# Kernel tuning notes

Hardware: AMD Instinct MI355X
Metric: run time of the kernel (lower is better)

Reference implementation:

```python
import jax, jax.numpy as jnp
import numpy as np

B, L, D = 4, 2048, 512
CHUNK = 64
EPS = 1e-5


def setup_inputs() -> dict:
    key = jax.random.key(0)
    kx, kw = jax.random.split(key)
    x = jax.random.normal(kx, (B, L, D), dtype=jnp.float32)
    W = jax.random.normal(kw, (D, D), dtype=jnp.float32) / np.float32(np.sqrt(D))
    return {
        "x": x,
        "W": W,
        "eta": jnp.asarray(0.01, jnp.float32),
        "lam_logit": jnp.asarray(np.log(0.99 / 0.01), jnp.float32),  # logit(0.99)
        "ln_gamma": jnp.ones((D,), jnp.float32),
        "ln_beta": jnp.zeros((D,), jnp.float32),
    }


def _gated_delta_scan(k, v, q, lam, beta):
    """Gated delta rule: S_t = lam*S_{t-1} + beta * k_t (x) (v_t - lam*S_{t-1}^T k_t);
    o_t = S_t^T q_t (scale=1.0, single head of dim D). k,v,q: [B,L,D] -> o: [B,L,D]."""
    b, l, d = k.shape
    nc = l // CHUNK

    def to_scan(t):  # [B,L,D] -> [nc, CHUNK, B, D]
        return t.transpose(1, 0, 2).reshape(nc, CHUNK, b, d)

    ks, vs, qs = to_scan(k), to_scan(v), to_scan(q)

    def step(S, inp):
        k_t, v_t, q_t = inp                      # each [B,D]
        S = lam * S                              # scalar decay exp(g), g = log(lam)
        v_err = beta * (v_t - jnp.einsum('bk,bkv->bv', k_t, S))
        S = S + k_t[:, :, None] * v_err[:, None, :]
        o_t = jnp.einsum('bk,bkv->bv', q_t, S)
        return S, o_t

    def chunk_body(S, ch):
        return jax.lax.scan(step, S, ch)

    S0 = jnp.zeros((b, d, d), k.dtype)
    _, o = jax.lax.scan(chunk_body, S0, (ks, vs, qs))  # o: [nc, CHUNK, B, D]
    return o.reshape(l, b, d).transpose(1, 0, 2)


def reference(x, W, eta, lam_logit, ln_gamma, ln_beta):
    lam = jax.nn.sigmoid(lam_logit)
    x_act = jnp.tanh(x)
    static_out = jnp.einsum('bld,ed->ble', x_act, W)  # torch Linear (no bias): x @ W.T
    # k = q = tanh(x), v = W @ tanh(x), g = log(lam), beta = eta
    o_dyn = _gated_delta_scan(x_act, static_out, x_act, lam, eta)
    y = static_out + o_dyn
    mu = jnp.mean(y, axis=-1, keepdims=True)
    var = jnp.var(y, axis=-1, keepdims=True)
    return (y - mu) * jax.lax.rsqrt(var + EPS) * ln_gamma + ln_beta
```

## Files before the change

### kernel.cpp

```cpp
#include <hip/hip_runtime.h>
#include <math.h>

#define BB 4
#define LL 2048
#define DD 512
#define CC 64
#define NC 32
#define VB 8
#define EPSF 1e-5f

typedef unsigned int u32;
typedef unsigned short u16;
typedef __attribute__((ext_vector_type(4))) u32 u32x4;
typedef __attribute__((ext_vector_type(4))) float f32x4;
typedef __attribute__((ext_vector_type(8))) __bf16 bf16x8;

__device__ __forceinline__ u16 f2bf(float f) {
  return __builtin_bit_cast(u16, (__bf16)f);
}
__device__ __forceinline__ int sx6(int s) { return (s ^ (s >> 3)) & 7; }
__device__ __forceinline__ bf16x8 ldf(const u16* p) {
  return __builtin_bit_cast(bf16x8, *(const u32x4*)p);
}
__device__ __forceinline__ bf16x8 bcv(u32x4 v) { return __builtin_bit_cast(bf16x8, v); }

__device__ __forceinline__ void gld16(u16* lds, const u16* g) {
  __builtin_amdgcn_global_load_lds(
      (const __attribute__((address_space(1))) u32*)g,
      (__attribute__((address_space(3))) u32*)lds, 16, 0, 0);
}
__device__ __forceinline__ void barrier_lgkm() {
  asm volatile("s_waitcnt lgkmcnt(0)" ::: "memory");
  __builtin_amdgcn_sched_barrier(0);
  __builtin_amdgcn_s_barrier();
  __builtin_amdgcn_sched_barrier(0);
}
__device__ __forceinline__ void barrier_all() {
  asm volatile("s_waitcnt vmcnt(0) lgkmcnt(0)" ::: "memory");
  __builtin_amdgcn_sched_barrier(0);
  __builtin_amdgcn_s_barrier();
  __builtin_amdgcn_sched_barrier(0);
}

__global__ __launch_bounds__(256) void k_cvtW(const float* __restrict__ W,
                                              u16* __restrict__ wbb) {
  int idx = (blockIdx.x * 256 + threadIdx.x) * 8;
  float4 a = *(const float4*)(W + idx);
  float4 b = *(const float4*)(W + idx + 4);
  float v[8] = {a.x, a.y, a.z, a.w, b.x, b.y, b.z, b.w};
  u32x4 pk;
#pragma unroll
  for (int j = 0; j < 4; ++j)
    pk[j] = (u32)f2bf(v[2 * j]) | ((u32)f2bf(v[2 * j + 1]) << 16);
  *(u32x4*)(wbb + idx) = pk;
}

__global__ __launch_bounds__(256) void k_prep3(const float* __restrict__ x,
                                               const float* __restrict__ eta_p,
                                               const float* __restrict__ ll_p,
                                               u16* __restrict__ kbs,
                                               u16* __restrict__ tbs,
                                               u16* __restrict__ tcs,
                                               u16* __restrict__ p1g,
                                               u16* __restrict__ p2g,
                                               u16* __restrict__ kbt) {
  __shared__ __align__(16) u16 Kl[CC * DD];
  __shared__ float Gl[64 * 64];
  __shared__ float Gs[64 * 64];
  __shared__ float Tl[64 * 65];
  __shared__ __align__(16) u16 MtL[64 * 64];
  __shared__ __align__(16) u16 TbT[64 * 64];
  __shared__ __align__(16) u16 TcT[64 * 64];
  __shared__ float pw[72];
  int bc = blockIdx.x;
  int b = bc >> 5, c = bc & 31;
  int tid = threadIdx.x;
  int wid = tid >> 6, lane = tid & 63;
  int lo = lane & 15, hi = lane >> 4;
  float beta = *eta_p;
  float lam = 1.f / (1.f + expf(-*ll_p));
  if (tid <= 64) pw[tid] = powf(lam, (float)tid);
  for (int i = tid; i < 64 * 65; i += 256) Tl[i] = 0.f;
  const float* xg = x + (size_t)(b * LL + c * CC) * DD;
  u16* kbs_c = kbs + (size_t)(b * LL + c * CC) * DD;
#pragma unroll
  for (int i = 0; i < 16; ++i) {
    int idx = tid + i * 256;
    int r = idx >> 6, k8 = (idx & 63) * 8;
    const float* xp = xg + (size_t)r * DD + k8;
    float4 a = *(const float4*)xp;
    float4 b4 = *(const float4*)(xp + 4);
    float v[8] = {a.x, a.y, a.z, a.w, b4.x, b4.y, b4.z, b4.w};
    u32x4 pk;
#pragma unroll
    for (int j = 0; j < 4; ++j)
      pk[j] = (u32)f2bf(tanhf(v[2 * j])) | ((u32)f2bf(tanhf(v[2 * j + 1])) << 16);
    int off = r * DD + (k8 ^ (sx6(r) << 3));
    *(u32x4*)(Kl + off) = pk;
    *(u32x4*)(kbs_c + off) = pk;
  }
  __syncthreads();
  {
    f32x4 acc[4] = {{0.f,0.f,0.f,0.f},{0.f,0.f,0.f,0.f},{0.f,0.f,0.f,0.f},{0.f,0.f,0.f,0.f}};
    int t = 16 * wid + lo;
    int mT = sx6(t) << 3;
#pragma unroll
    for (int kq = 0; kq < 16; ++kq) {
      int col = hi * 8 + kq * 32;
      bf16x8 aF = ldf(Kl + t * DD + (col ^ mT));
#pragma unroll
      for (int sb = 0; sb < 4; ++sb) {
        int s = 16 * sb + lo;
        bf16x8 bF = ldf(Kl + s * DD + (col ^ (sx6(s) << 3)));
        acc[sb] = __builtin_amdgcn_mfma_f32_16x16x32_bf16(aF, bF, acc[sb], 0, 0, 0);
      }
    }
#pragma unroll
    for (int sb = 0; sb < 4; ++sb)
#pragma unroll
      for (int r = 0; r < 4; ++r)
        Gl[(16 * wid + 4 * hi + r) * 64 + 16 * sb + lo] = acc[sb][r];
  }
  __syncthreads();
#pragma unroll
  for (int i = 0; i < 16; ++i) {
    int idx = tid + i * 256;
    int tq = idx >> 6, sq = idx & 63;
    Gs[idx] = (sq < tq) ? beta * pw[tq - sq] * Gl[idx] : 0.f;
  }
  __syncthreads();
  {
    int q = hi;
    int j = 16 * wid + lo;
    for (int t = 0; t < 64; ++t) {
      float ps = 0.f;
#pragma unroll
      for (int i = 0; i < 16; ++i) {
        int s = 16 * q + i;
        ps = fmaf(Gs[t * 64 + s], Tl[s * 65 + j], ps);
      }
      ps += __shfl_xor(ps, 16, 64);
      ps += __shfl_xor(ps, 32, 64);
      if (q == 0) Tl[t * 65 + j] = ((t == j) ? 1.f : 0.f) - ps;
    }
  }
  __syncthreads();
  u16* tbso = tbs + (size_t)bc * 4096;
  u16* tcso = tcs + (size_t)bc * 4096;
#pragma unroll
  for (int i = 0; i < 16; ++i) {
    int idx = tid + i * 256;
    int s = idx >> 6, r = idx & 63;
    float tv = Tl[s * 65 + r];
    float sc = pw[63 - s] * beta;
    tbso[idx] = f2bf(sc * tv);
    tcso[idx] = f2bf(-sc * pw[r + 1] * tv);
    int swz = r ^ (sx6(s) << 3);
    float mtv = (r < s) ? pw[s - r] * Gl[s * 64 + r]
                        : ((r == s) ? Gl[s * 64 + r] : 0.f);
    MtL[s * 64 + swz] = f2bf(mtv);
    float tvT = Tl[r * 65 + s];
    TbT[s * 64 + swz] = f2bf(beta * tvT);
    TcT[s * 64 + swz] = f2bf(-beta * pw[s + 1] * tvT);
  }
  __syncthreads();
  {
    f32x4 p1a[4], p2a[4];
#pragma unroll
    for (int rt = 0; rt < 4; ++rt) {
      p1a[rt] = (f32x4){0.f, 0.f, 0.f, 0.f};
      p2a[rt] = (f32x4){0.f, 0.f, 0.f, 0.f};
    }
    int srow = 16 * wid + lo;
    int aswz = sx6(srow) << 3;
#pragma unroll
    for (int km = 0; km < 2; ++km) {
      int mo = hi * 8 + km * 32;
      bf16x8 aF = ldf(MtL + srow * 64 + (mo ^ aswz));
#pragma unroll
      for (int rt = 0; rt < 4; ++rt) {
        int rrow = 16 * rt + lo;
        int bswz = sx6(rrow) << 3;
        p1a[rt] = __builtin_amdgcn_mfma_f32_16x16x32_bf16(
            aF, ldf(TbT + rrow * 64 + (mo ^ bswz)), p1a[rt], 0, 0, 0);
        p2a[rt] = __builtin_amdgcn_mfma_f32_16x16x32_bf16(
            aF, ldf(TcT + rrow * 64 + (mo ^ bswz)), p2a[rt], 0, 0, 0);
      }
    }
    u16* p1o = p1g + (size_t)bc * 4096;
    u16* p2o = p2g + (size_t)bc * 4096;
#pragma unroll
    for (int rt = 0; rt < 4; ++rt)
#pragma unroll
      for (int rg = 0; rg < 4; ++rg) {
        int s = 16 * wid + 4 * hi + rg;
        int r = 16 * rt + lo;
        float d1 = (s == r) ? 1.f : 0.f;
        float d2 = (s == r) ? pw[s + 1] : 0.f;
        p1o[s * 64 + r] = f2bf(p1a[rt][rg] + d1);
        p2o[s * 64 + r] = f2bf(p2a[rt][rg] + d2);
      }
  }
  u16* ktb = kbt + (size_t)bc * CC * DD;
#pragma unroll
  for (int rr = 0; rr < 2; ++rr) {
    int k = rr * 256 + tid;
    int kbase = k & ~7, klo = k & 7;
    int mk = sx6(k) << 3;
#pragma unroll
    for (int g = 0; g < 8; ++g) {
      u32 w4[4];
#pragma unroll
      for (int p = 0; p < 4; ++p) {
        int s0 = g * 8 + 2 * p;
        u16 e0 = Kl[s0 * DD + (kbase ^ (sx6(s0) << 3)) + klo];
        u16 e1 = Kl[(s0 + 1) * DD + (kbase ^ (sx6(s0 + 1) << 3)) + klo];
        w4[p] = (u32)e0 | ((u32)e1 << 16);
      }
      *(u32x4*)(ktb + (size_t)k * 64 + ((8 * g) ^ mk)) = (u32x4){w4[0], w4[1], w4[2], w4[3]};
    }
  }
}

__global__ __launch_bounds__(512, 2) void k_scanC(const u16* __restrict__ kbs,
                                                  const u16* __restrict__ kbt,
                                                  const u16* __restrict__ wbb,
                                                  const u16* __restrict__ tbs,
                                                  const u16* __restrict__ tcs,
                                                  const u16* __restrict__ p1g,
                                                  const u16* __restrict__ p2g,
                                                  const float* __restrict__ ll_p,
                                                  float* __restrict__ y) {
  __shared__ __align__(16) u16 Sb[16 * DD];
  __shared__ __align__(16) u16 Ut2[2][16 * 64];
  __shared__ __align__(16) u16 Vt2[2][16 * 64];
  __shared__ __align__(16) u16 Ws[16 * 64];

  int b = blockIdx.x >> 6;
  int vb = blockIdx.x & 63;
  int v0 = vb * VB;
  int tid = threadIdx.x;
  int wid = tid >> 6, lane = tid & 63;
  int wq = wid & 3, kh = wid >> 2;
  int lo = lane & 15, hi = lane >> 4;
  int sidx = 16 * wq + lo;
  int mS = sx6(sidx) << 3;
  int mLo = sx6(lo) << 3;
  int kOff = kh * 256;

  float lam = 1.f / (1.f + expf(-*ll_p));
  float lam64 = powf(lam, 64.f);

  {
    u32x4 z = {0u, 0u, 0u, 0u};
    ((u32x4*)Sb)[tid] = z;
    if (tid < 256) {
      ((u32x4*)Ut2)[tid] = z;
      ((u32x4*)Vt2)[tid] = z;
    }
    if (tid < 128) ((u32x4*)Ws)[tid] = z;
    if (wid < 8 && wid >= 0) {}
    if (wid < 8) {
      u32x4 wrow = *(const u32x4*)(wbb + (size_t)(v0 + wid) * DD + lane * 8);
      *(u32x4*)(Sb + (size_t)(8 + wid) * DD + ((lane * 8) ^ (sx6(8 + wid) << 3))) = wrow;
    }
  }
  const u16* kb_b = kbs + (size_t)b * LL * DD;
  float* yb = y + (size_t)b * LL * DD;

  u32x4 kB[8];
#pragma unroll
  for (int kq = 0; kq < 8; ++kq)
    kB[kq] = *(const u32x4*)(kb_b + (size_t)sidx * DD +
                             ((kOff + hi * 8 + kq * 32) ^ mS));
  u32x4 kt0[4], kt1[4], fA0, fA1, fB0, fB1;
  {
    const u16* ktc = kbt + (size_t)(b * NC + 0) * CC * DD;
#pragma unroll
    for (int t = 0; t < 4; ++t) {
      int k = 16 * (4 * wid + t) + lo;
      const u16* rowp = ktc + (size_t)k * 64;
      int m = sx6(k) << 3;
      kt0[t] = *(const u32x4*)(rowp + ((8 * hi) ^ m));
      kt1[t] = *(const u32x4*)(rowp + ((8 * hi + 32) ^ m));
    }
    size_t tbase = ((size_t)(b * NC + 0) * 64 + sidx) * 64 + hi * 8;
    const u16* mA = (kh == 0) ? tbs : p1g;
    const u16* mB = (kh == 0) ? tcs : p2g;
    fA0 = *(const u32x4*)(mA + tbase);
    fA1 = *(const u32x4*)(mA + tbase + 32);
    fB0 = *(const u32x4*)(mB + tbase);
    fB1 = *(const u32x4*)(mB + tbase + 32);
  }
  f32x4 Sa[4];
#pragma unroll
  for (int t = 0; t < 4; ++t) Sa[t] = (f32x4){0.f, 0.f, 0.f, 0.f};
  barrier_all();

  for (int c = 0; c < NC; ++c) {
    {
      f32x4 A0 = {0.f,0.f,0.f,0.f}, A1 = {0.f,0.f,0.f,0.f};
#pragma unroll
      for (int kq = 0; kq < 8; ++kq) {
        int col = kOff + hi * 8 + kq * 32;
        bf16x8 sA = ldf(Sb + lo * DD + (col ^ mLo));
        if (kq & 1) A1 = __builtin_amdgcn_mfma_f32_16x16x32_bf16(sA, bcv(kB[kq]), A1, 0, 0, 0);
        else        A0 = __builtin_amdgcn_mfma_f32_16x16x32_bf16(sA, bcv(kB[kq]), A0, 0, 0, 0);
      }
      f32x4 F = A0 + A1;
      if (hi < 2) {
#pragma unroll
        for (int r = 0; r < 4; ++r) {
          int m = 4 * hi + r;
          Ut2[kh][m * 64 + (sidx ^ (sx6(m) << 3))] = f2bf(F[r]);
        }
      } else {
#pragma unroll
        for (int r = 0; r < 4; ++r) {
          int m = 4 * hi + r - 8;
          Vt2[kh][m * 64 + (sidx ^ (sx6(m) << 3))] = f2bf(F[r]);
        }
      }
    }
    if (c + 1 < NC) {
      const u16* src = kb_b + ((size_t)(c + 1) * CC + sidx) * DD;
#pragma unroll
      for (int kq = 0; kq < 8; ++kq)
        kB[kq] = *(const u32x4*)(src + ((kOff + hi * 8 + kq * 32) ^ mS));
    }
    barrier_lgkm();
    {
      f32x4 Wa0 = {0.f,0.f,0.f,0.f}, Wa1 = {0.f,0.f,0.f,0.f};
#pragma unroll
      for (int h = 0; h < 2; ++h) {
        bf16x8 vf0 = ldf(Vt2[h] + lo * 64 + ((hi * 8) ^ mLo));
        bf16x8 vf1 = ldf(Vt2[h] + lo * 64 + ((hi * 8 + 32) ^ mLo));
        bf16x8 uf0 = ldf(Ut2[h] + lo * 64 + ((hi * 8) ^ mLo));
        bf16x8 uf1 = ldf(Ut2[h] + lo * 64 + ((hi * 8 + 32) ^ mLo));
        Wa0 = __builtin_amdgcn_mfma_f32_16x16x32_bf16(vf0, bcv(fA0), Wa0, 0, 0, 0);
        Wa1 = __builtin_amdgcn_mfma_f32_16x16x32_bf16(vf1, bcv(fA1), Wa1, 0, 0, 0);
        Wa0 = __builtin_amdgcn_mfma_f32_16x16x32_bf16(uf0, bcv(fB0), Wa0, 0, 0, 0);
        Wa1 = __builtin_amdgcn_mfma_f32_16x16x32_bf16(uf1, bcv(fB1), Wa1, 0, 0, 0);
      }
      f32x4 Wa = Wa0 + Wa1;
      if (kh == 0) {
        if (hi < 2) {
#pragma unroll
          for (int r = 0; r < 4; ++r) {
            int v = 4 * hi + r;
            Ws[v * 64 + (sidx ^ (sx6(v) << 3))] = f2bf(Wa[r]);
          }
        }
      } else {
        if (hi < 2) {
          float4 yo = make_float4(Wa[0], Wa[1], Wa[2], Wa[3]);
          *(float4*)(yb + (size_t)(c * CC + sidx) * DD + v0 + 4 * hi) = yo;
        }
      }
    }
    barrier_lgkm();
    {
      bf16x8 ws0 = ldf(Ws + lo * 64 + ((hi * 8) ^ mLo));
      bf16x8 ws1 = ldf(Ws + lo * 64 + ((hi * 8 + 32) ^ mLo));
#pragma unroll
      for (int t = 0; t < 4; ++t) {
        f32x4 acc = Sa[t] * lam64;
        acc = __builtin_amdgcn_mfma_f32_16x16x32_bf16(ws0, bcv(kt0[t]), acc, 0, 0, 0);
        acc = __builtin_amdgcn_mfma_f32_16x16x32_bf16(ws1, bcv(kt1[t]), acc, 0, 0, 0);
        Sa[t] = acc;
      }
      if (hi < 2) {
#pragma unroll
        for (int t = 0; t < 4; ++t) {
          int kc = 16 * (4 * wid + t) + lo;
#pragma unroll
          for (int r = 0; r < 4; ++r) {
            int v = 4 * hi + r;
            Sb[v * DD + (kc ^ (sx6(v) << 3))] = f2bf(Sa[t][r]);
          }
        }
      }
    }
    if (c + 1 < NC) {
      const u16* ktc = kbt + (size_t)(b * NC + c + 1) * CC * DD;
#pragma unroll
      for (int t = 0; t < 4; ++t) {
        int k = 16 * (4 * wid + t) + lo;
        const u16* rowp = ktc + (size_t)k * 64;
        int m = sx6(k) << 3;
        kt0[t] = *(const u32x4*)(rowp + ((8 * hi) ^ m));
        kt1[t] = *(const u32x4*)(rowp + ((8 * hi + 32) ^ m));
      }
      size_t tbase = ((size_t)(b * NC + c + 1) * 64 + sidx) * 64 + hi * 8;
      const u16* mA = (kh == 0) ? tbs : p1g;
      const u16* mB = (kh == 0) ? tcs : p2g;
      fA0 = *(const u32x4*)(mA + tbase);
      fA1 = *(const u32x4*)(mA + tbase + 32);
      fB0 = *(const u32x4*)(mB + tbase);
      fB1 = *(const u32x4*)(mB + tbase + 32);
    }
    barrier_lgkm();
  }
}

__global__ __launch_bounds__(256) void k_ln(float* __restrict__ y,
                                            const float* __restrict__ gamma,
                                            const float* __restrict__ lbeta) {
  int row = blockIdx.x * 4 + (threadIdx.x >> 6);
  int lane = threadIdx.x & 63;
  float* yr = y + (size_t)row * DD + lane * 8;
  float4 a = *(const float4*)yr;
  float4 b = *(const float4*)(yr + 4);
  float v[8] = {a.x, a.y, a.z, a.w, b.x, b.y, b.z, b.w};
  float s = 0.f, ss = 0.f;
#pragma unroll
  for (int j = 0; j < 8; ++j) {
    s += v[j];
    ss = fmaf(v[j], v[j], ss);
  }
#pragma unroll
  for (int m = 1; m < 64; m <<= 1) {
    s += __shfl_xor(s, m, 64);
    ss += __shfl_xor(ss, m, 64);
  }
  float mu = s * (1.f / DD);
  float var = ss * (1.f / DD) - mu * mu;
  float inv = rsqrtf(var + EPSF);
  const float* gp = gamma + lane * 8;
  const float* bp = lbeta + lane * 8;
  float4 g0 = *(const float4*)gp;
  float4 g1 = *(const float4*)(gp + 4);
  float4 b0 = *(const float4*)bp;
  float4 b1 = *(const float4*)(bp + 4);
  float g[8] = {g0.x, g0.y, g0.z, g0.w, g1.x, g1.y, g1.z, g1.w};
  float bb[8] = {b0.x, b0.y, b0.z, b0.w, b1.x, b1.y, b1.z, b1.w};
#pragma unroll
  for (int j = 0; j < 8; ++j) v[j] = (v[j] - mu) * inv * g[j] + bb[j];
  *(float4*)yr = make_float4(v[0], v[1], v[2], v[3]);
  *(float4*)(yr + 4) = make_float4(v[4], v[5], v[6], v[7]);
}

extern "C" void kernel_launch(void* const* d_in, const int* in_sizes, int n_in,
                              void* d_out, int out_size, void* d_ws, size_t ws_size,
                              hipStream_t stream) {
  const float* x     = (const float*)d_in[0];
  const float* W     = (const float*)d_in[1];
  const float* eta   = (const float*)d_in[2];
  const float* ll    = (const float*)d_in[3];
  const float* gamma = (const float*)d_in[4];
  const float* lbeta = (const float*)d_in[5];
  float* out = (float*)d_out;

  u16* kbs = (u16*)d_ws;
  u16* kbt = kbs + (size_t)BB * LL * DD;
  u16* wbb = kbt + (size_t)BB * LL * DD;
  u16* tbs = wbb + (size_t)DD * DD;
  u16* tcs = tbs + (size_t)BB * NC * 64 * 64;
  u16* p1g = tcs + (size_t)BB * NC * 64 * 64;
  u16* p2g = p1g + (size_t)BB * NC * 64 * 64;

  k_cvtW<<<128, 256, 0, stream>>>(W, wbb);
  k_prep3<<<BB * NC, 256, 0, stream>>>(x, eta, ll, kbs, tbs, tcs, p1g, p2g, kbt);
  k_scanC<<<256, 512, 0, stream>>>(kbs, kbt, wbb, tbs, tcs, p1g, p2g, ll, out);
  k_ln<<<2048, 256, 0, stream>>>(out, gamma, lbeta);
}
```

Before: 146.4 us.

## Split prep kernel into wide tanh/convert, transpose, and chunk-matrix kernels

```diff
diff --git a/kernel.cpp b/kernel.cpp
--- a/kernel.cpp
+++ b/kernel.cpp
@@ -42,28 +42,89 @@
   __builtin_amdgcn_sched_barrier(0);
 }
 
-__global__ __launch_bounds__(256) void k_cvtW(const float* __restrict__ W,
-                                              u16* __restrict__ wbb) {
-  int idx = (blockIdx.x * 256 + threadIdx.x) * 8;
-  float4 a = *(const float4*)(W + idx);
-  float4 b = *(const float4*)(W + idx + 4);
-  float v[8] = {a.x, a.y, a.z, a.w, b.x, b.y, b.z, b.w};
-  u32x4 pk;
-#pragma unroll
-  for (int j = 0; j < 4; ++j)
-    pk[j] = (u32)f2bf(v[2 * j]) | ((u32)f2bf(v[2 * j + 1]) << 16);
-  *(u32x4*)(wbb + idx) = pk;
-}
-
-__global__ __launch_bounds__(256) void k_prep3(const float* __restrict__ x,
+__global__ __launch_bounds__(256) void k_pre(const float* __restrict__ x,
+                                             const float* __restrict__ W,
+                                             u16* __restrict__ kbs,
+                                             u16* __restrict__ wbb) {
+  int blk = blockIdx.x;
+  if (blk < 2048) {
+    int row  = blk * 4 + (threadIdx.x >> 6);
+    int lane = threadIdx.x & 63;
+    const float* xr = x + (size_t)row * DD + lane * 8;
+    float4 a = *(const float4*)xr;
+    float4 b = *(const float4*)(xr + 4);
+    float v[8] = {a.x, a.y, a.z, a.w, b.x, b.y, b.z, b.w};
+    u32x4 pk;
+#pragma unroll
+    for (int j = 0; j < 4; ++j) {
+      u16 h0 = f2bf(tanhf(v[2 * j]));
+      u16 h1 = f2bf(tanhf(v[2 * j + 1]));
+      pk[j] = (u32)h0 | ((u32)h1 << 16);
+    }
+    int s = row & 63;
+    int k0 = (lane * 8) ^ (sx6(s) << 3);
+    *(u32x4*)(kbs + (size_t)row * DD + k0) = pk;
+  } else {
+    int idx = ((blk - 2048) * 256 + threadIdx.x) * 8;
+    float4 a = *(const float4*)(W + idx);
+    float4 b = *(const float4*)(W + idx + 4);
+    float v[8] = {a.x, a.y, a.z, a.w, b.x, b.y, b.z, b.w};
+    u32x4 pk;
+#pragma unroll
+    for (int j = 0; j < 4; ++j)
+      pk[j] = (u32)f2bf(v[2 * j]) | ((u32)f2bf(v[2 * j + 1]) << 16);
+    *(u32x4*)(wbb + idx) = pk;
+  }
+}
+
+__global__ __launch_bounds__(256) void k_trans(const u16* __restrict__ kbs,
+                                               u16* __restrict__ kbt) {
+  __shared__ __align__(16) u16 Ls[16 * 520];
+  int bc = blockIdx.x >> 2;
+  int q = blockIdx.x & 3;
+  int b = bc >> 5, c = bc & 31;
+  int tid = threadIdx.x;
+  int s0 = q * 16;
+  const u16* kbs_c = kbs + (size_t)(b * LL + c * CC) * DD;
+  u16* ktb = kbt + (size_t)bc * CC * DD;
+#pragma unroll
+  for (int i = 0; i < 4; ++i) {
+    int idx = tid + i * 256;
+    int r = idx >> 6;
+    int k8 = (idx & 63) * 8;
+    int s = s0 + r;
+    u32x4 v = *(const u32x4*)(kbs_c + (size_t)s * DD + (k8 ^ (sx6(s) << 3)));
+    *(u32x4*)&Ls[r * 520 + k8] = v;
+  }
+  __syncthreads();
+#pragma unroll
+  for (int kk = 0; kk < 2; ++kk) {
+    int k = tid * 2 + kk;
+    int mk = sx6(k) << 3;
+#pragma unroll
+    for (int g2 = 0; g2 < 2; ++g2) {
+      int g = q * 2 + g2;
+      u32 w4[4];
+#pragma unroll
+      for (int p = 0; p < 4; ++p) {
+        int sL = g2 * 8 + 2 * p;
+        u16 e0 = Ls[sL * 520 + k];
+        u16 e1 = Ls[(sL + 1) * 520 + k];
+        w4[p] = (u32)e0 | ((u32)e1 << 16);
+      }
+      *(u32x4*)(ktb + (size_t)k * 64 + ((8 * g) ^ mk)) =
+          (u32x4){w4[0], w4[1], w4[2], w4[3]};
+    }
+  }
+}
+
+__global__ __launch_bounds__(256) void k_prep4(const u16* __restrict__ kbs,
                                                const float* __restrict__ eta_p,
                                                const float* __restrict__ ll_p,
-                                               u16* __restrict__ kbs,
                                                u16* __restrict__ tbs,
                                                u16* __restrict__ tcs,
                                                u16* __restrict__ p1g,
-                                               u16* __restrict__ p2g,
-                                               u16* __restrict__ kbt) {
+                                               u16* __restrict__ p2g) {
   __shared__ __align__(16) u16 Kl[CC * DD];
   __shared__ float Gl[64 * 64];
   __shared__ float Gs[64 * 64];
@@ -81,24 +142,10 @@
   float lam = 1.f / (1.f + expf(-*ll_p));
   if (tid <= 64) pw[tid] = powf(lam, (float)tid);
   for (int i = tid; i < 64 * 65; i += 256) Tl[i] = 0.f;
-  const float* xg = x + (size_t)(b * LL + c * CC) * DD;
-  u16* kbs_c = kbs + (size_t)(b * LL + c * CC) * DD;
-#pragma unroll
-  for (int i = 0; i < 16; ++i) {
-    int idx = tid + i * 256;
-    int r = idx >> 6, k8 = (idx & 63) * 8;
-    const float* xp = xg + (size_t)r * DD + k8;
-    float4 a = *(const float4*)xp;
-    float4 b4 = *(const float4*)(xp + 4);
-    float v[8] = {a.x, a.y, a.z, a.w, b4.x, b4.y, b4.z, b4.w};
-    u32x4 pk;
-#pragma unroll
-    for (int j = 0; j < 4; ++j)
-      pk[j] = (u32)f2bf(tanhf(v[2 * j])) | ((u32)f2bf(tanhf(v[2 * j + 1])) << 16);
-    int off = r * DD + (k8 ^ (sx6(r) << 3));
-    *(u32x4*)(Kl + off) = pk;
-    *(u32x4*)(kbs_c + off) = pk;
-  }
+  const u16* Kg = kbs + (size_t)(b * LL + c * CC) * DD;
+#pragma unroll
+  for (int i = 0; i < 16; ++i)
+    gld16(Kl + (size_t)(i * 256 + tid) * 8, Kg + (size_t)(i * 256 + tid) * 8);
   __syncthreads();
   {
     f32x4 acc[4] = {{0.f,0.f,0.f,0.f},{0.f,0.f,0.f,0.f},{0.f,0.f,0.f,0.f},{0.f,0.f,0.f,0.f}};
@@ -201,25 +248,6 @@
         p2o[s * 64 + r] = f2bf(p2a[rt][rg] + d2);
       }
   }
-  u16* ktb = kbt + (size_t)bc * CC * DD;
-#pragma unroll
-  for (int rr = 0; rr < 2; ++rr) {
-    int k = rr * 256 + tid;
-    int kbase = k & ~7, klo = k & 7;
-    int mk = sx6(k) << 3;
-#pragma unroll
-    for (int g = 0; g < 8; ++g) {
-      u32 w4[4];
-#pragma unroll
-      for (int p = 0; p < 4; ++p) {
-        int s0 = g * 8 + 2 * p;
-        u16 e0 = Kl[s0 * DD + (kbase ^ (sx6(s0) << 3)) + klo];
-        u16 e1 = Kl[(s0 + 1) * DD + (kbase ^ (sx6(s0 + 1) << 3)) + klo];
-        w4[p] = (u32)e0 | ((u32)e1 << 16);
-      }
-      *(u32x4*)(ktb + (size_t)k * 64 + ((8 * g) ^ mk)) = (u32x4){w4[0], w4[1], w4[2], w4[3]};
-    }
-  }
 }
 
 __global__ __launch_bounds__(512, 2) void k_scanC(const u16* __restrict__ kbs,
@@ -259,7 +287,6 @@
       ((u32x4*)Vt2)[tid] = z;
     }
     if (tid < 128) ((u32x4*)Ws)[tid] = z;
-    if (wid < 8 && wid >= 0) {}
     if (wid < 8) {
       u32x4 wrow = *(const u32x4*)(wbb + (size_t)(v0 + wid) * DD + lane * 8);
       *(u32x4*)(Sb + (size_t)(8 + wid) * DD + ((lane * 8) ^ (sx6(8 + wid) << 3))) = wrow;
@@ -300,6 +327,7 @@
   for (int c = 0; c < NC; ++c) {
     {
       f32x4 A0 = {0.f,0.f,0.f,0.f}, A1 = {0.f,0.f,0.f,0.f};
+      __builtin_amdgcn_s_setprio(1);
 #pragma unroll
       for (int kq = 0; kq < 8; ++kq) {
         int col = kOff + hi * 8 + kq * 32;
@@ -307,6 +335,7 @@
         if (kq & 1) A1 = __builtin_amdgcn_mfma_f32_16x16x32_bf16(sA, bcv(kB[kq]), A1, 0, 0, 0);
         else        A0 = __builtin_amdgcn_mfma_f32_16x16x32_bf16(sA, bcv(kB[kq]), A0, 0, 0, 0);
       }
+      __builtin_amdgcn_s_setprio(0);
       f32x4 F = A0 + A1;
       if (hi < 2) {
 #pragma unroll
@@ -331,6 +360,7 @@
     barrier_lgkm();
     {
       f32x4 Wa0 = {0.f,0.f,0.f,0.f}, Wa1 = {0.f,0.f,0.f,0.f};
+      __builtin_amdgcn_s_setprio(1);
 #pragma unroll
       for (int h = 0; h < 2; ++h) {
         bf16x8 vf0 = ldf(Vt2[h] + lo * 64 + ((hi * 8) ^ mLo));
@@ -342,6 +372,7 @@
         Wa0 = __builtin_amdgcn_mfma_f32_16x16x32_bf16(uf0, bcv(fB0), Wa0, 0, 0, 0);
         Wa1 = __builtin_amdgcn_mfma_f32_16x16x32_bf16(uf1, bcv(fB1), Wa1, 0, 0, 0);
       }
+      __builtin_amdgcn_s_setprio(0);
       f32x4 Wa = Wa0 + Wa1;
       if (kh == 0) {
         if (hi < 2) {
@@ -362,6 +393,7 @@
     {
       bf16x8 ws0 = ldf(Ws + lo * 64 + ((hi * 8) ^ mLo));
       bf16x8 ws1 = ldf(Ws + lo * 64 + ((hi * 8 + 32) ^ mLo));
+      __builtin_amdgcn_s_setprio(1);
 #pragma unroll
       for (int t = 0; t < 4; ++t) {
         f32x4 acc = Sa[t] * lam64;
@@ -369,6 +401,7 @@
         acc = __builtin_amdgcn_mfma_f32_16x16x32_bf16(ws1, bcv(kt1[t]), acc, 0, 0, 0);
         Sa[t] = acc;
       }
+      __builtin_amdgcn_s_setprio(0);
       if (hi < 2) {
 #pragma unroll
         for (int t = 0; t < 4; ++t) {
@@ -459,8 +492,9 @@
   u16* p1g = tcs + (size_t)BB * NC * 64 * 64;
   u16* p2g = p1g + (size_t)BB * NC * 64 * 64;
 
-  k_cvtW<<<128, 256, 0, stream>>>(W, wbb);
-  k_prep3<<<BB * NC, 256, 0, stream>>>(x, eta, ll, kbs, tbs, tcs, p1g, p2g, kbt);
+  k_pre<<<2176, 256, 0, stream>>>(x, W, kbs, wbb);
+  k_trans<<<512, 256, 0, stream>>>(kbs, kbt);
+  k_prep4<<<BB * NC, 256, 0, stream>>>(kbs, eta, ll, tbs, tcs, p1g, p2g);
   k_scanC<<<256, 512, 0, stream>>>(kbs, kbt, wbb, tbs, tcs, p1g, p2g, ll, out);
   k_ln<<<2048, 256, 0, stream>>>(out, gamma, lbeta);
 }
```

Result: faster. 137.6 us (-6.0%).

## Split preprocessing into wide tanh/transpose kernel and 512-thread chunk-matrix kernel

Applied to the files above, without the earlier changes.

```diff
diff --git a/kernel.cpp b/kernel.cpp
--- a/kernel.cpp
+++ b/kernel.cpp
@@ -42,28 +42,78 @@
   __builtin_amdgcn_sched_barrier(0);
 }
 
-__global__ __launch_bounds__(256) void k_cvtW(const float* __restrict__ W,
-                                              u16* __restrict__ wbb) {
-  int idx = (blockIdx.x * 256 + threadIdx.x) * 8;
-  float4 a = *(const float4*)(W + idx);
-  float4 b = *(const float4*)(W + idx + 4);
-  float v[8] = {a.x, a.y, a.z, a.w, b.x, b.y, b.z, b.w};
-  u32x4 pk;
-#pragma unroll
-  for (int j = 0; j < 4; ++j)
-    pk[j] = (u32)f2bf(v[2 * j]) | ((u32)f2bf(v[2 * j + 1]) << 16);
-  *(u32x4*)(wbb + idx) = pk;
-}
-
-__global__ __launch_bounds__(256) void k_prep3(const float* __restrict__ x,
+__global__ __launch_bounds__(256) void k_pre2(const float* __restrict__ x,
+                                              const float* __restrict__ W,
+                                              u16* __restrict__ kbs,
+                                              u16* __restrict__ wbb,
+                                              u16* __restrict__ kbt) {
+  __shared__ __align__(16) u16 Ls[16 * 520];
+  int blk = blockIdx.x;
+  int tid = threadIdx.x;
+  if (blk < 512) {
+    int bc = blk >> 2;
+    int q = blk & 3;
+    int b = bc >> 5, c = bc & 31;
+    int s0 = q * 16;
+    const float* xg = x + (size_t)(b * LL + c * CC + s0) * DD;
+    u16* kbs_c = kbs + (size_t)(b * LL + c * CC + s0) * DD;
+#pragma unroll
+    for (int i = 0; i < 4; ++i) {
+      int idx = tid + i * 256;
+      int r = idx >> 6, k8 = (idx & 63) * 8;
+      const float* xp = xg + (size_t)r * DD + k8;
+      float4 a = *(const float4*)xp;
+      float4 b4 = *(const float4*)(xp + 4);
+      float v[8] = {a.x, a.y, a.z, a.w, b4.x, b4.y, b4.z, b4.w};
+      u32x4 pk;
+#pragma unroll
+      for (int j = 0; j < 4; ++j)
+        pk[j] = (u32)f2bf(tanhf(v[2 * j])) | ((u32)f2bf(tanhf(v[2 * j + 1])) << 16);
+      int s = s0 + r;
+      *(u32x4*)(kbs_c + (size_t)r * DD + (k8 ^ (sx6(s) << 3))) = pk;
+      *(u32x4*)&Ls[r * 520 + k8] = pk;
+    }
+    __syncthreads();
+    u16* ktb = kbt + (size_t)bc * CC * DD;
+#pragma unroll
+    for (int kk = 0; kk < 2; ++kk) {
+      int k = tid * 2 + kk;
+      int mk = sx6(k) << 3;
+#pragma unroll
+      for (int g2 = 0; g2 < 2; ++g2) {
+        int g = q * 2 + g2;
+        u32 w4[4];
+#pragma unroll
+        for (int p = 0; p < 4; ++p) {
+          int sL = g2 * 8 + 2 * p;
+          u16 e0 = Ls[sL * 520 + k];
+          u16 e1 = Ls[(sL + 1) * 520 + k];
+          w4[p] = (u32)e0 | ((u32)e1 << 16);
+        }
+        *(u32x4*)(ktb + (size_t)k * 64 + ((8 * g) ^ mk)) =
+            (u32x4){w4[0], w4[1], w4[2], w4[3]};
+      }
+    }
+  } else {
+    int idx = ((blk - 512) * 256 + tid) * 8;
+    float4 a = *(const float4*)(W + idx);
+    float4 b = *(const float4*)(W + idx + 4);
+    float v[8] = {a.x, a.y, a.z, a.w, b.x, b.y, b.z, b.w};
+    u32x4 pk;
+#pragma unroll
+    for (int j = 0; j < 4; ++j)
+      pk[j] = (u32)f2bf(v[2 * j]) | ((u32)f2bf(v[2 * j + 1]) << 16);
+    *(u32x4*)(wbb + idx) = pk;
+  }
+}
+
+__global__ __launch_bounds__(512) void k_prep5(const u16* __restrict__ kbs,
                                                const float* __restrict__ eta_p,
                                                const float* __restrict__ ll_p,
-                                               u16* __restrict__ kbs,
                                                u16* __restrict__ tbs,
                                                u16* __restrict__ tcs,
                                                u16* __restrict__ p1g,
-                                               u16* __restrict__ p2g,
-                                               u16* __restrict__ kbt) {
+                                               u16* __restrict__ p2g) {
   __shared__ __align__(16) u16 Kl[CC * DD];
   __shared__ float Gl[64 * 64];
   __shared__ float Gs[64 * 64];
@@ -76,37 +126,24 @@
   int b = bc >> 5, c = bc & 31;
   int tid = threadIdx.x;
   int wid = tid >> 6, lane = tid & 63;
+  int wq2 = wid & 3, kh2 = wid >> 2;
   int lo = lane & 15, hi = lane >> 4;
   float beta = *eta_p;
   float lam = 1.f / (1.f + expf(-*ll_p));
   if (tid <= 64) pw[tid] = powf(lam, (float)tid);
-  for (int i = tid; i < 64 * 65; i += 256) Tl[i] = 0.f;
-  const float* xg = x + (size_t)(b * LL + c * CC) * DD;
-  u16* kbs_c = kbs + (size_t)(b * LL + c * CC) * DD;
-#pragma unroll
-  for (int i = 0; i < 16; ++i) {
-    int idx = tid + i * 256;
-    int r = idx >> 6, k8 = (idx & 63) * 8;
-    const float* xp = xg + (size_t)r * DD + k8;
-    float4 a = *(const float4*)xp;
-    float4 b4 = *(const float4*)(xp + 4);
-    float v[8] = {a.x, a.y, a.z, a.w, b4.x, b4.y, b4.z, b4.w};
-    u32x4 pk;
-#pragma unroll
-    for (int j = 0; j < 4; ++j)
-      pk[j] = (u32)f2bf(tanhf(v[2 * j])) | ((u32)f2bf(tanhf(v[2 * j + 1])) << 16);
-    int off = r * DD + (k8 ^ (sx6(r) << 3));
-    *(u32x4*)(Kl + off) = pk;
-    *(u32x4*)(kbs_c + off) = pk;
-  }
+  for (int i = tid; i < 64 * 65; i += 512) Tl[i] = 0.f;
+  const u16* Kg = kbs + (size_t)(b * LL + c * CC) * DD;
+#pragma unroll
+  for (int i = 0; i < 8; ++i)
+    gld16(Kl + (size_t)(i * 512 + tid) * 8, Kg + (size_t)(i * 512 + tid) * 8);
   __syncthreads();
   {
     f32x4 acc[4] = {{0.f,0.f,0.f,0.f},{0.f,0.f,0.f,0.f},{0.f,0.f,0.f,0.f},{0.f,0.f,0.f,0.f}};
-    int t = 16 * wid + lo;
+    int t = 16 * wq2 + lo;
     int mT = sx6(t) << 3;
 #pragma unroll
-    for (int kq = 0; kq < 16; ++kq) {
-      int col = hi * 8 + kq * 32;
+    for (int kq = 0; kq < 8; ++kq) {
+      int col = kh2 * 256 + hi * 8 + kq * 32;
       bf16x8 aF = ldf(Kl + t * DD + (col ^ mT));
 #pragma unroll
       for (int sb = 0; sb < 4; ++sb) {
@@ -115,21 +152,24 @@
         acc[sb] = __builtin_amdgcn_mfma_f32_16x16x32_bf16(aF, bF, acc[sb], 0, 0, 0);
       }
     }
+    float* Gp = kh2 ? Gs : Gl;
 #pragma unroll
     for (int sb = 0; sb < 4; ++sb)
 #pragma unroll
       for (int r = 0; r < 4; ++r)
-        Gl[(16 * wid + 4 * hi + r) * 64 + 16 * sb + lo] = acc[sb][r];
+        Gp[(16 * wq2 + 4 * hi + r) * 64 + 16 * sb + lo] = acc[sb][r];
   }
   __syncthreads();
 #pragma unroll
-  for (int i = 0; i < 16; ++i) {
-    int idx = tid + i * 256;
+  for (int i = 0; i < 8; ++i) {
+    int idx = tid + i * 512;
     int tq = idx >> 6, sq = idx & 63;
-    Gs[idx] = (sq < tq) ? beta * pw[tq - sq] * Gl[idx] : 0.f;
+    float g = Gl[idx] + Gs[idx];
+    Gl[idx] = g;
+    Gs[idx] = (sq < tq) ? beta * pw[tq - sq] * g : 0.f;
   }
   __syncthreads();
-  {
+  if (tid < 256) {
     int q = hi;
     int j = 16 * wid + lo;
     for (int t = 0; t < 64; ++t) {
@@ -148,8 +188,8 @@
   u16* tbso = tbs + (size_t)bc * 4096;
   u16* tcso = tcs + (size_t)bc * 4096;
 #pragma unroll
-  for (int i = 0; i < 16; ++i) {
-    int idx = tid + i * 256;
+  for (int i = 0; i < 8; ++i) {
+    int idx = tid + i * 512;
     int s = idx >> 6, r = idx & 63;
     float tv = Tl[s * 65 + r];
     float sc = pw[63 - s] * beta;
@@ -165,14 +205,12 @@
   }
   __syncthreads();
   {
-    f32x4 p1a[4], p2a[4];
-#pragma unroll
-    for (int rt = 0; rt < 4; ++rt) {
-      p1a[rt] = (f32x4){0.f, 0.f, 0.f, 0.f};
-      p2a[rt] = (f32x4){0.f, 0.f, 0.f, 0.f};
-    }
-    int srow = 16 * wid + lo;
+    f32x4 pa[4];
+#pragma unroll
+    for (int rt = 0; rt < 4; ++rt) pa[rt] = (f32x4){0.f, 0.f, 0.f, 0.f};
+    int srow = 16 * wq2 + lo;
     int aswz = sx6(srow) << 3;
+    const u16* Bt = kh2 ? TcT : TbT;
 #pragma unroll
     for (int km = 0; km < 2; ++km) {
       int mo = hi * 8 + km * 32;
@@ -181,44 +219,21 @@
       for (int rt = 0; rt < 4; ++rt) {
         int rrow = 16 * rt + lo;
         int bswz = sx6(rrow) << 3;
-        p1a[rt] = __builtin_amdgcn_mfma_f32_16x16x32_bf16(
-            aF, ldf(TbT + rrow * 64 + (mo ^ bswz)), p1a[rt], 0, 0, 0);
-        p2a[rt] = __builtin_amdgcn_mfma_f32_16x16x32_bf16(
-            aF, ldf(TcT + rrow * 64 + (mo ^ bswz)), p2a[rt], 0, 0, 0);
-      }
-    }
-    u16* p1o = p1g + (size_t)bc * 4096;
-    u16* p2o = p2g + (size_t)bc * 4096;
+        pa[rt] = __builtin_amdgcn_mfma_f32_16x16x32_bf16(
+            aF, ldf(Bt + rrow * 64 + (mo ^ bswz)), pa[rt], 0, 0, 0);
+      }
+    }
+    u16* po = (kh2 ? p2g : p1g) + (size_t)bc * 4096;
 #pragma unroll
     for (int rt = 0; rt < 4; ++rt)
 #pragma unroll
       for (int rg = 0; rg < 4; ++rg) {
-        int s = 16 * wid + 4 * hi + rg;
+        int s = 16 * wq2 + 4 * hi + rg;
         int r = 16 * rt + lo;
-        float d1 = (s == r) ? 1.f : 0.f;
-        float d2 = (s == r) ? pw[s + 1] : 0.f;
-        p1o[s * 64 + r] = f2bf(p1a[rt][rg] + d1);
-        p2o[s * 64 + r] = f2bf(p2a[rt][rg] + d2);
-      }
-  }
-  u16* ktb = kbt + (size_t)bc * CC * DD;
-#pragma unroll
-  for (int rr = 0; rr < 2; ++rr) {
-    int k = rr * 256 + tid;
-    int kbase = k & ~7, klo = k & 7;
-    int mk = sx6(k) << 3;
-#pragma unroll
-    for (int g = 0; g < 8; ++g) {
-      u32 w4[4];
-#pragma unroll
-      for (int p = 0; p < 4; ++p) {
-        int s0 = g * 8 + 2 * p;
-        u16 e0 = Kl[s0 * DD + (kbase ^ (sx6(s0) << 3)) + klo];
-        u16 e1 = Kl[(s0 + 1) * DD + (kbase ^ (sx6(s0 + 1) << 3)) + klo];
-        w4[p] = (u32)e0 | ((u32)e1 << 16);
-      }
-      *(u32x4*)(ktb + (size_t)k * 64 + ((8 * g) ^ mk)) = (u32x4){w4[0], w4[1], w4[2], w4[3]};
-    }
+        float d = kh2 ? ((s == r) ? pw[s + 1] : 0.f)
+                      : ((s == r) ? 1.f : 0.f);
+        po[s * 64 + r] = f2bf(pa[rt][rg] + d);
+      }
   }
 }
 
@@ -259,7 +274,6 @@
       ((u32x4*)Vt2)[tid] = z;
     }
     if (tid < 128) ((u32x4*)Ws)[tid] = z;
-    if (wid < 8 && wid >= 0) {}
     if (wid < 8) {
       u32x4 wrow = *(const u32x4*)(wbb + (size_t)(v0 + wid) * DD + lane * 8);
       *(u32x4*)(Sb + (size_t)(8 + wid) * DD + ((lane * 8) ^ (sx6(8 + wid) << 3))) = wrow;
@@ -459,8 +473,8 @@
   u16* p1g = tcs + (size_t)BB * NC * 64 * 64;
   u16* p2g = p1g + (size_t)BB * NC * 64 * 64;
 
-  k_cvtW<<<128, 256, 0, stream>>>(W, wbb);
-  k_prep3<<<BB * NC, 256, 0, stream>>>(x, eta, ll, kbs, tbs, tcs, p1g, p2g, kbt);
+  k_pre2<<<640, 256, 0, stream>>>(x, W, kbs, wbb, kbt);
+  k_prep5<<<BB * NC, 512, 0, stream>>>(kbs, eta, ll, tbs, tcs, p1g, p2g);
   k_scanC<<<256, 512, 0, stream>>>(kbs, kbt, wbb, tbs, tcs, p1g, p2g, ll, out);
   k_ln<<<2048, 256, 0, stream>>>(out, gamma, lbeta);
 }
```

After: 131.3 us (median of 3 runs). -10.3%, faster.
